# Kernel tuning notes

Hardware: AMD Instinct MI355X
Metric: run time of the kernel (lower is better)

Reference implementation:

```python
import jax, jax.numpy as jnp
import numpy as np

N = 10000
E = 160000
D = 512
EDGE_DIM = 128
L = 3
LN_EPS = 1e-5


def setup_inputs() -> dict:
    key = jax.random.key(0)
    ks = jax.random.split(key, 16)
    s = 0.02
    return {
        "x": jax.random.normal(ks[0], (N, D), dtype=jnp.float32),
        "edge_index": jax.random.randint(ks[1], (2, E), 0, N, dtype=jnp.int64),
        "edge_attr": jax.random.normal(ks[2], (E, EDGE_DIM), dtype=jnp.float32),
        # per-layer GINEConv edge projection Linear(edge_dim -> d_in); here d_in == D for all layers
        "We": jax.random.normal(ks[3], (L, EDGE_DIM, D), dtype=jnp.float32) * s,
        "be": jnp.zeros((L, D), dtype=jnp.float32),
        "eps": jnp.zeros((L,), dtype=jnp.float32),  # train_eps=True, init 0
        # per-layer MLP: Linear(D->D), ReLU, Linear(D->D)
        "W1": jax.random.normal(ks[4], (L, D, D), dtype=jnp.float32) * s,
        "b1": jnp.zeros((L, D), dtype=jnp.float32),
        "W2": jax.random.normal(ks[5], (L, D, D), dtype=jnp.float32) * s,
        "b2": jnp.zeros((L, D), dtype=jnp.float32),
        # per-layer LayerNorm
        "gamma": jnp.ones((L, D), dtype=jnp.float32),
        "beta": jnp.zeros((L, D), dtype=jnp.float32),
        # final Linear(D->D)
        "Wf": jax.random.normal(ks[6], (D, D), dtype=jnp.float32) * s,
        "bf": jnp.zeros((D,), dtype=jnp.float32),
    }


def reference(x, edge_index, edge_attr, We, be, eps, W1, b1, W2, b2, gamma, beta, Wf, bf):
    src = edge_index[0]  # x_j (source)
    dst = edge_index[1]  # aggregation target i
    n = x.shape[0]
    h = x
    for l in range(L):
        # GINEConv message: relu(x_j + lin(edge_attr)), scatter-add at dst
        e = jax.nn.relu(h[src] + edge_attr @ We[l] + be[l])  # [E, D]
        agg = jax.ops.segment_sum(e, dst, num_segments=n)     # [N, D]
        g = (1.0 + eps[l]) * h + agg
        # 2-layer MLP
        g = jax.nn.relu(g @ W1[l] + b1[l]) @ W2[l] + b2[l]
        # ReLU then LayerNorm (dropout p=0)
        g = jax.nn.relu(g)
        mu = jnp.mean(g, axis=-1, keepdims=True)
        var = jnp.mean(jnp.square(g - mu), axis=-1, keepdims=True)
        h = (g - mu) * jax.lax.rsqrt(var + LN_EPS) * gamma[l] + beta[l]
    return h @ Wf + bf
```

## Files before the change

### kernel.cpp

```cpp
#include <hip/hip_runtime.h>

#define NN 10000
#define EE 160000
#define DD 512
#define EDIM 128
#define LLAYERS 3
#define LN_EPS 1e-5f

typedef __attribute__((ext_vector_type(8))) short bf16x8;
typedef __attribute__((ext_vector_type(4))) float f32x4;

__device__ __forceinline__ unsigned short f2b(float f) {
    union { float f; unsigned u; } v; v.f = f;
    unsigned r = (v.u + 0x7fffu + ((v.u >> 16) & 1u)) >> 16;
    return (unsigned short)r;
}
__device__ __forceinline__ float b2f(unsigned short s) {
    union { unsigned u; float f; } v; v.u = ((unsigned)s) << 16;
    return v.f;
}
__device__ __forceinline__ unsigned short f2h(float f) {
    _Float16 h = (_Float16)f;
    unsigned short u; __builtin_memcpy(&u, &h, 2);
    return u;
}
__device__ __forceinline__ float h2f(unsigned short u) {
    _Float16 h; __builtin_memcpy(&h, &u, 2);
    return (float)h;
}

__global__ __launch_bounds__(256) void hist_kernel(
    const int* __restrict__ dstv, int* __restrict__ deg)
{
    int e = blockIdx.x * 256 + threadIdx.x;
    if (e < EE) atomicAdd(&deg[dstv[e]], 1);
}

__global__ __launch_bounds__(256) void scan_kernel(
    const int* __restrict__ deg, int* __restrict__ base, int* __restrict__ cursor)
{
    __shared__ int sums[256];
    const int t = threadIdx.x;
    const int CH = 40;
    int lo = t * CH;
    int hi = lo + CH; if (hi > NN) hi = NN;
    int s = 0;
    for (int i = lo; i < hi; i++) s += deg[i];
    sums[t] = s;
    __syncthreads();
    for (int off = 1; off < 256; off <<= 1) {
        int v = (t >= off) ? sums[t - off] : 0;
        __syncthreads();
        sums[t] += v;
        __syncthreads();
    }
    int run = (t == 0) ? 0 : sums[t - 1];
    for (int i = lo; i < hi; i++) {
        base[i] = run; cursor[i] = run;
        run += deg[i];
    }
}

__global__ __launch_bounds__(256) void scatter_kernel(
    const int* __restrict__ srcv, const int* __restrict__ dstv,
    int* __restrict__ cursor,
    int* __restrict__ ssrc, int* __restrict__ sdst, int* __restrict__ perm)
{
    int e = blockIdx.x * 256 + threadIdx.x;
    if (e < EE) {
        int d = dstv[e];
        int pos = atomicAdd(&cursor[d], 1);
        ssrc[pos] = srcv[e];
        sdst[pos] = d;
        perm[pos] = e;
    }
}

__global__ __launch_bounds__(256) void transpose_bf16_kernel(
    const float* __restrict__ src, unsigned short* __restrict__ dst, int K, int N)
{
    __shared__ float t[32][33];
    const int x = threadIdx.x & 31;
    const int y = threadIdx.x >> 5;
    const int bn = blockIdx.x * 32;
    const int bk = blockIdx.y * 32;
    #pragma unroll
    for (int j = 0; j < 32; j += 8)
        t[y + j][x] = src[(size_t)(bk + y + j) * N + bn + x];
    __syncthreads();
    #pragma unroll
    for (int j = 0; j < 32; j += 8)
        dst[(size_t)(bn + y + j) * K + bk + x] = f2b(t[x][y + j]);
}

__global__ __launch_bounds__(256) void cvt_bf16_kernel(
    const float* __restrict__ src, unsigned short* __restrict__ dst)
{
    int i = blockIdx.x * 256 + threadIdx.x;
    float4 v = ((const float4*)src)[i];
    uint2 o;
    o.x = (unsigned)f2b(v.x) | ((unsigned)f2b(v.y) << 16);
    o.y = (unsigned)f2b(v.z) | ((unsigned)f2b(v.w) << 16);
    ((uint2*)dst)[i] = o;
}

__global__ __launch_bounds__(256) void gather_cvt_kernel(
    const float* __restrict__ ea, const int* __restrict__ perm,
    unsigned short* __restrict__ out, int elo)
{
    int i = blockIdx.x * 256 + threadIdx.x;
    int r = i >> 5, c4 = (i & 31) * 4;
    const float* p = ea + (size_t)perm[elo + r] * EDIM + c4;
    float4 v = *(const float4*)p;
    uint2 o;
    o.x = (unsigned)f2b(v.x) | ((unsigned)f2b(v.y) << 16);
    o.y = (unsigned)f2b(v.z) | ((unsigned)f2b(v.w) << 16);
    *(uint2*)&out[(size_t)r * EDIM + c4] = o;
}

#define MEP 136
__global__ __launch_bounds__(256) void msg_gemm(
    const unsigned short* __restrict__ Abf,
    const unsigned short* __restrict__ WeT,
    const float* __restrict__ be,
    unsigned short* __restrict__ msg)
{
    __shared__ unsigned short sA[128 * MEP];

    const int tid  = threadIdx.x;
    const int c0   = blockIdx.x * 128;
    const int e0   = blockIdx.y * 128;
    const int w    = tid >> 6;
    const int lane = tid & 63;
    const int quad = lane >> 4;
    const int l16  = lane & 15;
    const int mh   = (w & 1) * 64;
    const int nsl  = (w >> 1) * 64;

    for (int i = tid; i < 128 * 16; i += 256) {
        int r = i >> 4, seg = i & 15;
        *(uint4*)&sA[r * MEP + seg * 8] =
            *(const uint4*)&Abf[(size_t)(e0 + r) * EDIM + seg * 8];
    }
    __syncthreads();

    f32x4 acc[4][4];
    #pragma unroll
    for (int mr = 0; mr < 4; mr++)
        #pragma unroll
        for (int nb = 0; nb < 4; nb++)
            acc[mr][nb] = (f32x4){0.f, 0.f, 0.f, 0.f};

    #pragma unroll
    for (int ks = 0; ks < 4; ks++) {
        const int ko = ks * 32 + quad * 8;
        bf16x8 a[4];
        #pragma unroll
        for (int mr = 0; mr < 4; mr++)
            a[mr] = *(const bf16x8*)&sA[(mh + mr * 16 + l16) * MEP + ko];
        bf16x8 b[4];
        #pragma unroll
        for (int nb = 0; nb < 4; nb++)
            b[nb] = *(const bf16x8*)&WeT[(size_t)(c0 + nsl + nb * 16 + l16) * EDIM + ko];
        #pragma unroll
        for (int mr = 0; mr < 4; mr++)
            #pragma unroll
            for (int nb = 0; nb < 4; nb++)
                acc[mr][nb] = __builtin_amdgcn_mfma_f32_16x16x32_bf16(a[mr], b[nb], acc[mr][nb], 0, 0, 0);
    }

    #pragma unroll
    for (int mr = 0; mr < 4; mr++) {
        const int rb = e0 + mh + mr * 16 + quad * 4;
        #pragma unroll
        for (int nb = 0; nb < 4; nb++) {
            const int c = c0 + nsl + nb * 16 + l16;
            const float bv = be[c];
            const f32x4 v = acc[mr][nb];
            #pragma unroll
            for (int reg = 0; reg < 4; reg++)
                msg[(size_t)(rb + reg) * DD + c] = f2h(v[reg] + bv);
        }
    }
}

__global__ __launch_bounds__(256) void agg_kernel(
    const unsigned short* __restrict__ h_bf,
    const unsigned short* __restrict__ msg,
    const int* __restrict__ ssrc,
    const int* __restrict__ basep,
    const int* __restrict__ degp,
    const float* __restrict__ epsp,
    float* __restrict__ aggp,
    unsigned short* __restrict__ aprime,
    int elo, int ehi, int first, int last)
{
    const int d  = blockIdx.x;
    const int b0 = basep[d];
    const int b1 = b0 + degp[d];
    int lo = b0 > elo ? b0 : elo;
    int hi = b1 < ehi ? b1 : ehi;
    if (!first && !last && lo >= hi) return;

    const int t  = threadIdx.x;
    const int c2 = t * 2;

    float a0 = 0.f, a1 = 0.f;
    if (!first) {
        float2 pv = *(const float2*)&aggp[(size_t)d * DD + c2];
        a0 = pv.x; a1 = pv.y;
    }
    for (int p = lo; p < hi; p++) {
        const int s = ssrc[p];
        unsigned mv = *(const unsigned*)&msg[(size_t)(p - elo) * DD + c2];
        unsigned hv = *(const unsigned*)&h_bf[(size_t)s * DD + c2];
        a0 += fmaxf(h2f((unsigned short)(mv & 0xffffu)) + b2f((unsigned short)(hv & 0xffffu)), 0.f);
        a1 += fmaxf(h2f((unsigned short)(mv >> 16))     + b2f((unsigned short)(hv >> 16)),     0.f);
    }
    if (last) {
        const float es = 1.0f + epsp[0];
        unsigned hv = *(const unsigned*)&h_bf[(size_t)d * DD + c2];
        unsigned o = (unsigned)f2b(es * b2f((unsigned short)(hv & 0xffffu)) + a0)
                   | ((unsigned)f2b(es * b2f((unsigned short)(hv >> 16))    + a1) << 16);
        *(unsigned*)&aprime[(size_t)d * DD + c2] = o;
    } else {
        *(float2*)&aggp[(size_t)d * DD + c2] = make_float2(a0, a1);
    }
}

#define GPITCH 136
template <bool RELU, bool OUTBF>
__global__ __launch_bounds__(256) void mfma_gemm(
    const unsigned short* __restrict__ A,
    const unsigned short* __restrict__ WT,
    const float* __restrict__ bias,
    void* __restrict__ Cout, int M)
{
    __shared__ unsigned short sA[64 * GPITCH];
    __shared__ unsigned short sB[128 * GPITCH];

    const int tid  = threadIdx.x;
    const int m0   = blockIdx.x * 64;
    const int c0   = blockIdx.y * 128;
    const int w    = tid >> 6;
    const int lane = tid & 63;
    const int quad = lane >> 4;
    const int l16  = lane & 15;
    const int mh   = (w & 1) * 32;
    const int nsl  = (w >> 1) * 64;

    f32x4 acc[2][4];
    #pragma unroll
    for (int mr = 0; mr < 2; mr++)
        #pragma unroll
        for (int nb = 0; nb < 4; nb++)
            acc[mr][nb] = (f32x4){0.f, 0.f, 0.f, 0.f};

    for (int kc = 0; kc < DD; kc += 128) {
        __syncthreads();
        for (int i = tid; i < 64 * 16; i += 256) {
            int r = i >> 4, seg = i & 15;
            int gm = m0 + r;
            uint4 v = make_uint4(0u, 0u, 0u, 0u);
            if (gm < M)
                v = *(const uint4*)&A[(size_t)gm * DD + kc + seg * 8];
            *(uint4*)&sA[r * GPITCH + seg * 8] = v;
        }
        for (int i = tid; i < 128 * 16; i += 256) {
            int r = i >> 4, seg = i & 15;
            *(uint4*)&sB[r * GPITCH + seg * 8] =
                *(const uint4*)&WT[(size_t)(c0 + r) * DD + kc + seg * 8];
        }
        __syncthreads();
        #pragma unroll
        for (int ks = 0; ks < 4; ks++) {
            const int ko = ks * 32 + quad * 8;
            bf16x8 a0 = *(const bf16x8*)&sA[(mh + l16) * GPITCH + ko];
            bf16x8 a1 = *(const bf16x8*)&sA[(mh + 16 + l16) * GPITCH + ko];
            bf16x8 b[4];
            #pragma unroll
            for (int nb = 0; nb < 4; nb++)
                b[nb] = *(const bf16x8*)&sB[(nsl + nb * 16 + l16) * GPITCH + ko];
            #pragma unroll
            for (int nb = 0; nb < 4; nb++) {
                acc[0][nb] = __builtin_amdgcn_mfma_f32_16x16x32_bf16(a0, b[nb], acc[0][nb], 0, 0, 0);
                acc[1][nb] = __builtin_amdgcn_mfma_f32_16x16x32_bf16(a1, b[nb], acc[1][nb], 0, 0, 0);
            }
        }
    }

    #pragma unroll
    for (int mr = 0; mr < 2; mr++) {
        const int rbase = m0 + mh + mr * 16 + quad * 4;
        #pragma unroll
        for (int nb = 0; nb < 4; nb++) {
            const int c = c0 + nsl + nb * 16 + l16;
            const float bv = bias[c];
            const f32x4 v = acc[mr][nb];
            #pragma unroll
            for (int reg = 0; reg < 4; reg++) {
                int gm = rbase + reg;
                if (gm < M) {
                    float val = v[reg] + bv;
                    if (RELU) val = fmaxf(val, 0.f);
                    if (OUTBF) ((unsigned short*)Cout)[(size_t)gm * DD + c] = f2b(val);
                    else       ((float*)Cout)[(size_t)gm * DD + c] = val;
                }
            }
        }
    }
}

__global__ __launch_bounds__(256) void relu_ln_kernel(
    const unsigned short* __restrict__ g2,
    const float* __restrict__ gamma,
    const float* __restrict__ beta,
    unsigned short* __restrict__ hout)
{
    __shared__ float ss[4], ssq[4];
    const int row = blockIdx.x;
    const int tid = threadIdx.x;
    const unsigned short* gr = g2 + (size_t)row * DD;

    float v0 = fmaxf(b2f(gr[tid]), 0.f);
    float v1 = fmaxf(b2f(gr[tid + 256]), 0.f);
    float s  = v0 + v1;
    float sq = v0 * v0 + v1 * v1;
    #pragma unroll
    for (int off = 32; off > 0; off >>= 1) {
        s  += __shfl_down(s, off);
        sq += __shfl_down(sq, off);
    }
    const int wave = tid >> 6;
    const int lane = tid & 63;
    if (lane == 0) { ss[wave] = s; ssq[wave] = sq; }
    __syncthreads();
    if (tid == 0) {
        float S  = ss[0] + ss[1] + ss[2] + ss[3];
        float SQ = ssq[0] + ssq[1] + ssq[2] + ssq[3];
        float mu = S * (1.f / 512.f);
        float var = SQ * (1.f / 512.f) - mu * mu;
        ss[0]  = mu;
        ssq[0] = rsqrtf(var + LN_EPS);
    }
    __syncthreads();
    float mu = ss[0], rstd = ssq[0];
    hout[(size_t)row * DD + tid] =
        f2b((v0 - mu) * rstd * gamma[tid] + beta[tid]);
    hout[(size_t)row * DD + tid + 256] =
        f2b((v1 - mu) * rstd * gamma[tid + 256] + beta[tid + 256]);
}

extern "C" void kernel_launch(void* const* d_in, const int* in_sizes, int n_in,
                              void* d_out, int out_size, void* d_ws, size_t ws_size,
                              hipStream_t stream)
{
    (void)in_sizes; (void)n_in; (void)out_size;

    const float* x          = (const float*)d_in[0];
    const int*   edge_index = (const int*)d_in[1];
    const float* edge_attr  = (const float*)d_in[2];
    const float* We         = (const float*)d_in[3];
    const float* be         = (const float*)d_in[4];
    const float* eps        = (const float*)d_in[5];
    const float* W1         = (const float*)d_in[6];
    const float* b1         = (const float*)d_in[7];
    const float* W2         = (const float*)d_in[8];
    const float* b2         = (const float*)d_in[9];
    const float* gamma      = (const float*)d_in[10];
    const float* beta       = (const float*)d_in[11];
    const float* Wf         = (const float*)d_in[12];
    const float* bf         = (const float*)d_in[13];

    unsigned short* h_bf   = (unsigned short*)d_ws;
    unsigned short* aprime = h_bf + (size_t)NN * DD;
    unsigned short* t1     = aprime + (size_t)NN * DD;
    unsigned short* t2     = t1 + (size_t)NN * DD;
    unsigned short* WeT    = t2 + (size_t)NN * DD;
    unsigned short* W1T    = WeT + (size_t)LLAYERS * DD * EDIM;
    unsigned short* W2T    = W1T + (size_t)LLAYERS * DD * DD;
    unsigned short* WfT    = W2T + (size_t)LLAYERS * DD * DD;
    int* deg    = (int*)(WfT + (size_t)DD * DD);
    int* basep  = deg + NN;
    int* cursor = basep + NN;
    int* ssrc   = cursor + NN;
    int* sdst   = ssrc + EE;
    int* perm   = sdst + EE;
    float* aggp = (float*)(perm + EE);
    unsigned short* ea_hf = (unsigned short*)(aggp + (size_t)NN * DD);

    size_t used = (size_t)((unsigned char*)ea_hf - (unsigned char*)d_ws);
    size_t rem  = ws_size > used ? ws_size - used : 0;
    const size_t EA_FULL  = (size_t)EE * EDIM * 2;
    const size_t MSG_FULL = (size_t)EE * DD * 2;
    int ea_full; long long capE;
    if (rem >= EA_FULL + MSG_FULL) {
        ea_full = 1; capE = EE;
    } else if (rem >= EA_FULL + (size_t)32 * 1024 * 1024) {
        ea_full = 1;
        capE = (long long)((rem - EA_FULL) / ((size_t)DD * 2)) & ~127LL;
    } else {
        ea_full = 0;
        capE = (long long)(rem / ((size_t)(EDIM + DD) * 2)) & ~127LL;
        if (capE < 128) capE = 128;
    }
    if (capE > EE) capE = EE;
    unsigned short* msg = ea_hf + (ea_full ? (size_t)EE * EDIM : (size_t)capE * EDIM);

    const int* srcv = edge_index;
    const int* dstv = edge_index + EE;

    hipMemsetAsync(deg, 0, NN * sizeof(int), stream);
    hist_kernel<<<dim3((EE + 255) / 256), 256, 0, stream>>>(dstv, deg);
    scan_kernel<<<dim3(1), 256, 0, stream>>>(deg, basep, cursor);
    scatter_kernel<<<dim3((EE + 255) / 256), 256, 0, stream>>>(
        srcv, dstv, cursor, ssrc, sdst, perm);

    cvt_bf16_kernel<<<dim3(NN * DD / 4 / 256), 256, 0, stream>>>(x, h_bf);
    for (int l = 0; l < LLAYERS; l++) {
        transpose_bf16_kernel<<<dim3(DD / 32, EDIM / 32), 256, 0, stream>>>(
            We + (size_t)l * EDIM * DD, WeT + (size_t)l * DD * EDIM, EDIM, DD);
        transpose_bf16_kernel<<<dim3(DD / 32, DD / 32), 256, 0, stream>>>(
            W1 + (size_t)l * DD * DD, W1T + (size_t)l * DD * DD, DD, DD);
        transpose_bf16_kernel<<<dim3(DD / 32, DD / 32), 256, 0, stream>>>(
            W2 + (size_t)l * DD * DD, W2T + (size_t)l * DD * DD, DD, DD);
    }
    transpose_bf16_kernel<<<dim3(DD / 32, DD / 32), 256, 0, stream>>>(Wf, WfT, DD, DD);

    if (ea_full)
        gather_cvt_kernel<<<dim3(EE / 8), 256, 0, stream>>>(edge_attr, perm, ea_hf, 0);

    dim3 ggrid((NN + 63) / 64, DD / 128);

    const int nch = (int)((EE + capE - 1) / capE);
    for (int l = 0; l < LLAYERS; l++) {
        for (int c = 0; c < nch; c++) {
            const int elo = (int)((long long)c * capE);
            const int cnt = (EE - elo < capE) ? (EE - elo) : (int)capE;
            if (!ea_full)
                gather_cvt_kernel<<<dim3(cnt / 8), 256, 0, stream>>>(edge_attr, perm, ea_hf, elo);
            const unsigned short* Ab = ea_full ? ea_hf + (size_t)elo * EDIM : ea_hf;
            msg_gemm<<<dim3(4, cnt / 128), 256, 0, stream>>>(
                Ab, WeT + (size_t)l * DD * EDIM, be + (size_t)l * DD, msg);
            agg_kernel<<<dim3(NN), 256, 0, stream>>>(
                h_bf, msg, ssrc, basep, deg, eps + l, aggp, aprime,
                elo, elo + cnt, c == 0 ? 1 : 0, c == nch - 1 ? 1 : 0);
        }
        mfma_gemm<true, true><<<ggrid, 256, 0, stream>>>(
            aprime, W1T + (size_t)l * DD * DD, b1 + (size_t)l * DD, t1, NN);
        mfma_gemm<false, true><<<ggrid, 256, 0, stream>>>(
            t1, W2T + (size_t)l * DD * DD, b2 + (size_t)l * DD, t2, NN);
        relu_ln_kernel<<<dim3(NN), 256, 0, stream>>>(
            t2, gamma + (size_t)l * DD, beta + (size_t)l * DD, h_bf);
    }
    mfma_gemm<false, false><<<ggrid, 256, 0, stream>>>(h_bf, WfT, bf, d_out, NN);
}
```

Baseline: 834.6 us.

## Stage msg output through LDS, unroll aggregation, retile node GEMMs to 64x64

The message GEMM now writes its fp16 results into shared memory and then stores them to global memory as coalesced 16-byte rows instead of scattered 2-byte writes. The aggregation loop is unrolled by four so more gathers of messages and source features are in flight at once. The node GEMMs are replaced by a 64x64 tile kernel that keeps only A in LDS and reads weight fragments straight from global/L2, giving more blocks and less LDS per block. The LayerNorm kernel now uses packed 32-bit loads and stores. These changes trade more redundant weight reads for higher occupancy and better store coalescing.

```diff
diff --git a/kernel.cpp b/kernel.cpp
--- a/kernel.cpp
+++ b/kernel.cpp
@@ -9,6 +9,7 @@
 
 typedef __attribute__((ext_vector_type(8))) short bf16x8;
 typedef __attribute__((ext_vector_type(4))) float f32x4;
+typedef __attribute__((ext_vector_type(4))) unsigned int u32x4;
 
 __device__ __forceinline__ unsigned short f2b(float f) {
     union { float f; unsigned u; } v; v.f = f;
@@ -119,6 +120,7 @@
 }
 
 #define MEP 136
+
 __global__ __launch_bounds__(256) void msg_gemm(
     const unsigned short* __restrict__ Abf,
     const unsigned short* __restrict__ WeT,
@@ -139,8 +141,8 @@
 
     for (int i = tid; i < 128 * 16; i += 256) {
         int r = i >> 4, seg = i & 15;
-        *(uint4*)&sA[r * MEP + seg * 8] =
-            *(const uint4*)&Abf[(size_t)(e0 + r) * EDIM + seg * 8];
+        *(u32x4*)&sA[r * MEP + seg * 8] =
+            *(const u32x4*)&Abf[(size_t)(e0 + r) * EDIM + seg * 8];
     }
     __syncthreads();
 
@@ -169,18 +171,25 @@
                 acc[mr][nb] = __builtin_amdgcn_mfma_f32_16x16x32_bf16(a[mr], b[nb], acc[mr][nb], 0, 0, 0);
     }
 
+    __syncthreads();
     #pragma unroll
     for (int mr = 0; mr < 4; mr++) {
-        const int rb = e0 + mh + mr * 16 + quad * 4;
+        const int lr = mh + mr * 16 + quad * 4;
         #pragma unroll
         for (int nb = 0; nb < 4; nb++) {
-            const int c = c0 + nsl + nb * 16 + l16;
-            const float bv = be[c];
+            const int lc = nsl + nb * 16 + l16;
+            const float bv = be[c0 + lc];
             const f32x4 v = acc[mr][nb];
             #pragma unroll
             for (int reg = 0; reg < 4; reg++)
-                msg[(size_t)(rb + reg) * DD + c] = f2h(v[reg] + bv);
+                sA[(lr + reg) * MEP + lc] = f2h(v[reg] + bv);
         }
+    }
+    __syncthreads();
+    for (int i = tid; i < 128 * 16; i += 256) {
+        int r = i >> 4, seg = i & 15;
+        *(u32x4*)&msg[(size_t)(e0 + r) * DD + c0 + seg * 8] =
+            *(const u32x4*)&sA[r * MEP + seg * 8];
     }
 }
 
@@ -210,7 +219,28 @@
         float2 pv = *(const float2*)&aggp[(size_t)d * DD + c2];
         a0 = pv.x; a1 = pv.y;
     }
-    for (int p = lo; p < hi; p++) {
+    int p = lo;
+    for (; p + 4 <= hi; p += 4) {
+        const int s0 = ssrc[p],     s1 = ssrc[p + 1];
+        const int s2 = ssrc[p + 2], s3 = ssrc[p + 3];
+        unsigned m0v = *(const unsigned*)&msg[(size_t)(p     - elo) * DD + c2];
+        unsigned m1v = *(const unsigned*)&msg[(size_t)(p + 1 - elo) * DD + c2];
+        unsigned m2v = *(const unsigned*)&msg[(size_t)(p + 2 - elo) * DD + c2];
+        unsigned m3v = *(const unsigned*)&msg[(size_t)(p + 3 - elo) * DD + c2];
+        unsigned h0v = *(const unsigned*)&h_bf[(size_t)s0 * DD + c2];
+        unsigned h1v = *(const unsigned*)&h_bf[(size_t)s1 * DD + c2];
+        unsigned h2v = *(const unsigned*)&h_bf[(size_t)s2 * DD + c2];
+        unsigned h3v = *(const unsigned*)&h_bf[(size_t)s3 * DD + c2];
+        a0 += fmaxf(h2f((unsigned short)(m0v & 0xffffu)) + b2f((unsigned short)(h0v & 0xffffu)), 0.f);
+        a1 += fmaxf(h2f((unsigned short)(m0v >> 16))     + b2f((unsigned short)(h0v >> 16)),     0.f);
+        a0 += fmaxf(h2f((unsigned short)(m1v & 0xffffu)) + b2f((unsigned short)(h1v & 0xffffu)), 0.f);
+        a1 += fmaxf(h2f((unsigned short)(m1v >> 16))     + b2f((unsigned short)(h1v >> 16)),     0.f);
+        a0 += fmaxf(h2f((unsigned short)(m2v & 0xffffu)) + b2f((unsigned short)(h2v & 0xffffu)), 0.f);
+        a1 += fmaxf(h2f((unsigned short)(m2v >> 16))     + b2f((unsigned short)(h2v >> 16)),     0.f);
+        a0 += fmaxf(h2f((unsigned short)(m3v & 0xffffu)) + b2f((unsigned short)(h3v & 0xffffu)), 0.f);
+        a1 += fmaxf(h2f((unsigned short)(m3v >> 16))     + b2f((unsigned short)(h3v >> 16)),     0.f);
+    }
+    for (; p < hi; p++) {
         const int s = ssrc[p];
         unsigned mv = *(const unsigned*)&msg[(size_t)(p - elo) * DD + c2];
         unsigned hv = *(const unsigned*)&h_bf[(size_t)s * DD + c2];
@@ -228,83 +258,75 @@
     }
 }
 
-#define GPITCH 136
-template <bool RELU, bool OUTBF>
-__global__ __launch_bounds__(256) void mfma_gemm(
+#define GP 136
+template <bool RELU, bool F32OUT>
+__global__ __launch_bounds__(256) void gemm64(
     const unsigned short* __restrict__ A,
     const unsigned short* __restrict__ WT,
     const float* __restrict__ bias,
     void* __restrict__ Cout, int M)
 {
-    __shared__ unsigned short sA[64 * GPITCH];
-    __shared__ unsigned short sB[128 * GPITCH];
+    __shared__ unsigned short sA[64 * GP];
 
     const int tid  = threadIdx.x;
-    const int m0   = blockIdx.x * 64;
-    const int c0   = blockIdx.y * 128;
+    const int c0   = blockIdx.x * 64;
+    const int m0   = blockIdx.y * 64;
     const int w    = tid >> 6;
     const int lane = tid & 63;
     const int quad = lane >> 4;
     const int l16  = lane & 15;
     const int mh   = (w & 1) * 32;
-    const int nsl  = (w >> 1) * 64;
-
-    f32x4 acc[2][4];
+    const int nsl  = (w >> 1) * 32;
+
+    f32x4 acc[2][2];
     #pragma unroll
     for (int mr = 0; mr < 2; mr++)
         #pragma unroll
-        for (int nb = 0; nb < 4; nb++)
+        for (int nb = 0; nb < 2; nb++)
             acc[mr][nb] = (f32x4){0.f, 0.f, 0.f, 0.f};
 
     for (int kc = 0; kc < DD; kc += 128) {
-        __syncthreads();
+        if (kc) __syncthreads();
+        #pragma unroll
         for (int i = tid; i < 64 * 16; i += 256) {
             int r = i >> 4, seg = i & 15;
             int gm = m0 + r;
-            uint4 v = make_uint4(0u, 0u, 0u, 0u);
+            u32x4 v = (u32x4){0u, 0u, 0u, 0u};
             if (gm < M)
-                v = *(const uint4*)&A[(size_t)gm * DD + kc + seg * 8];
-            *(uint4*)&sA[r * GPITCH + seg * 8] = v;
-        }
-        for (int i = tid; i < 128 * 16; i += 256) {
-            int r = i >> 4, seg = i & 15;
-            *(uint4*)&sB[r * GPITCH + seg * 8] =
-                *(const uint4*)&WT[(size_t)(c0 + r) * DD + kc + seg * 8];
+                v = *(const u32x4*)&A[(size_t)gm * DD + kc + seg * 8];
+            *(u32x4*)&sA[r * GP + seg * 8] = v;
         }
         __syncthreads();
         #pragma unroll
         for (int ks = 0; ks < 4; ks++) {
             const int ko = ks * 32 + quad * 8;
-            bf16x8 a0 = *(const bf16x8*)&sA[(mh + l16) * GPITCH + ko];
-            bf16x8 a1 = *(const bf16x8*)&sA[(mh + 16 + l16) * GPITCH + ko];
-            bf16x8 b[4];
-            #pragma unroll
-            for (int nb = 0; nb < 4; nb++)
-                b[nb] = *(const bf16x8*)&sB[(nsl + nb * 16 + l16) * GPITCH + ko];
-            #pragma unroll
-            for (int nb = 0; nb < 4; nb++) {
-                acc[0][nb] = __builtin_amdgcn_mfma_f32_16x16x32_bf16(a0, b[nb], acc[0][nb], 0, 0, 0);
-                acc[1][nb] = __builtin_amdgcn_mfma_f32_16x16x32_bf16(a1, b[nb], acc[1][nb], 0, 0, 0);
-            }
+            bf16x8 a0 = *(const bf16x8*)&sA[(mh + l16) * GP + ko];
+            bf16x8 a1 = *(const bf16x8*)&sA[(mh + 16 + l16) * GP + ko];
+            bf16x8 b0 = *(const bf16x8*)&WT[(size_t)(c0 + nsl + l16) * DD + kc + ko];
+            bf16x8 b1 = *(const bf16x8*)&WT[(size_t)(c0 + nsl + 16 + l16) * DD + kc + ko];
+            acc[0][0] = __builtin_amdgcn_mfma_f32_16x16x32_bf16(a0, b0, acc[0][0], 0, 0, 0);
+            acc[0][1] = __builtin_amdgcn_mfma_f32_16x16x32_bf16(a0, b1, acc[0][1], 0, 0, 0);
+            acc[1][0] = __builtin_amdgcn_mfma_f32_16x16x32_bf16(a1, b0, acc[1][0], 0, 0, 0);
+            acc[1][1] = __builtin_amdgcn_mfma_f32_16x16x32_bf16(a1, b1, acc[1][1], 0, 0, 0);
         }
     }
 
     #pragma unroll
     for (int mr = 0; mr < 2; mr++) {
-        const int rbase = m0 + mh + mr * 16 + quad * 4;
-        #pragma unroll
-        for (int nb = 0; nb < 4; nb++) {
-            const int c = c0 + nsl + nb * 16 + l16;
-            const float bv = bias[c];
+        const int rb = m0 + mh + mr * 16 + quad * 4;
+        #pragma unroll
+        for (int nb = 0; nb < 2; nb++) {
+            const int cc = c0 + nsl + nb * 16 + l16;
+            const float bv = bias[cc];
             const f32x4 v = acc[mr][nb];
             #pragma unroll
             for (int reg = 0; reg < 4; reg++) {
-                int gm = rbase + reg;
+                int gm = rb + reg;
                 if (gm < M) {
                     float val = v[reg] + bv;
                     if (RELU) val = fmaxf(val, 0.f);
-                    if (OUTBF) ((unsigned short*)Cout)[(size_t)gm * DD + c] = f2b(val);
-                    else       ((float*)Cout)[(size_t)gm * DD + c] = val;
+                    if (F32OUT) ((float*)Cout)[(size_t)gm * DD + cc] = val;
+                    else ((unsigned short*)Cout)[(size_t)gm * DD + cc] = f2b(val);
                 }
             }
         }
@@ -319,11 +341,12 @@
 {
     __shared__ float ss[4], ssq[4];
     const int row = blockIdx.x;
-    const int tid = threadIdx.x;
-    const unsigned short* gr = g2 + (size_t)row * DD;
-
-    float v0 = fmaxf(b2f(gr[tid]), 0.f);
-    float v1 = fmaxf(b2f(gr[tid + 256]), 0.f);
+    const int t   = threadIdx.x;
+    const unsigned* gr = (const unsigned*)(g2 + (size_t)row * DD);
+
+    unsigned gv = gr[t];
+    float v0 = fmaxf(b2f((unsigned short)(gv & 0xffffu)), 0.f);
+    float v1 = fmaxf(b2f((unsigned short)(gv >> 16)),     0.f);
     float s  = v0 + v1;
     float sq = v0 * v0 + v1 * v1;
     #pragma unroll
@@ -331,11 +354,11 @@
         s  += __shfl_down(s, off);
         sq += __shfl_down(sq, off);
     }
-    const int wave = tid >> 6;
-    const int lane = tid & 63;
+    const int wave = t >> 6;
+    const int lane = t & 63;
     if (lane == 0) { ss[wave] = s; ssq[wave] = sq; }
     __syncthreads();
-    if (tid == 0) {
+    if (t == 0) {
         float S  = ss[0] + ss[1] + ss[2] + ss[3];
         float SQ = ssq[0] + ssq[1] + ssq[2] + ssq[3];
         float mu = S * (1.f / 512.f);
@@ -345,10 +368,9 @@
     }
     __syncthreads();
     float mu = ss[0], rstd = ssq[0];
-    hout[(size_t)row * DD + tid] =
-        f2b((v0 - mu) * rstd * gamma[tid] + beta[tid]);
-    hout[(size_t)row * DD + tid + 256] =
-        f2b((v1 - mu) * rstd * gamma[tid + 256] + beta[tid + 256]);
+    unsigned o = (unsigned)f2b((v0 - mu) * rstd * gamma[2 * t] + beta[2 * t])
+               | ((unsigned)f2b((v1 - mu) * rstd * gamma[2 * t + 1] + beta[2 * t + 1]) << 16);
+    ((unsigned*)(hout + (size_t)row * DD))[t] = o;
 }
 
 extern "C" void kernel_launch(void* const* d_in, const int* in_sizes, int n_in,
@@ -430,7 +452,7 @@
     if (ea_full)
         gather_cvt_kernel<<<dim3(EE / 8), 256, 0, stream>>>(edge_attr, perm, ea_hf, 0);
 
-    dim3 ggrid((NN + 63) / 64, DD / 128);
+    dim3 ggrid64(DD / 64, (NN + 63) / 64);
 
     const int nch = (int)((EE + capE - 1) / capE);
     for (int l = 0; l < LLAYERS; l++) {
@@ -446,12 +468,12 @@
                 h_bf, msg, ssrc, basep, deg, eps + l, aggp, aprime,
                 elo, elo + cnt, c == 0 ? 1 : 0, c == nch - 1 ? 1 : 0);
         }
-        mfma_gemm<true, true><<<ggrid, 256, 0, stream>>>(
+        gemm64<true, false><<<ggrid64, 256, 0, stream>>>(
             aprime, W1T + (size_t)l * DD * DD, b1 + (size_t)l * DD, t1, NN);
-        mfma_gemm<false, true><<<ggrid, 256, 0, stream>>>(
+        gemm64<false, false><<<ggrid64, 256, 0, stream>>>(
             t1, W2T + (size_t)l * DD * DD, b2 + (size_t)l * DD, t2, NN);
         relu_ln_kernel<<<dim3(NN), 256, 0, stream>>>(
             t2, gamma + (size_t)l * DD, beta + (size_t)l * DD, h_bf);
     }
-    mfma_gemm<false, false><<<ggrid, 256, 0, stream>>>(h_bf, WfT, bf, d_out, NN);
-}
+    gemm64<false, true><<<ggrid64, 256, 0, stream>>>(h_bf, WfT, bf, d_out, NN);
+}
```

Result: slower. 859.3 us (+3.0%).
